# Kernel optimization log

Measured on AMD Instinct MI355X. Metric: run time of the kernel, lower is better.

## Reference

```python
import jax, jax.numpy as jnp
import numpy as np

D_MODEL = 1024
D_K = 64
MAX_LEN = 10000
SCALE = float(np.sqrt(2 * D_K))  # TUPE scale sqrt(2*d_k)


def setup_inputs() -> dict:
    key = jax.random.key(0)
    kq, kk, kv, kpe, kuq, kuk = jax.random.split(key, 6)
    b, s = 4, 2048
    q = jax.random.normal(kq, (b, s, D_MODEL), dtype=jnp.float32)
    k = jax.random.normal(kk, (b, s, D_MODEL), dtype=jnp.float32)
    v = jax.random.normal(kv, (b, s, D_MODEL), dtype=jnp.float32)
    # learned PE, uniform(-0.1, 0.1) as in the source
    pe = jax.random.uniform(kpe, (MAX_LEN, D_MODEL), minval=-0.1, maxval=0.1, dtype=jnp.float32)
    # U_q / U_k: Linear(d_model, d_model, bias=False); store as [in, out] so x @ W matches torch x @ W.T convention after transpose choice
    lim = 1.0 / np.sqrt(D_MODEL)
    Uq = jax.random.uniform(kuq, (D_MODEL, D_MODEL), minval=-lim, maxval=lim, dtype=jnp.float32)
    Uk = jax.random.uniform(kuk, (D_MODEL, D_MODEL), minval=-lim, maxval=lim, dtype=jnp.float32)
    return {"q": q, "k": k, "v": v, "pe": pe, "Uq": Uq, "Uk": Uk}


def reference(q, k, v, pe, Uq, Uk):
    b, len_q, d_model = q.shape
    len_k = k.shape[1]
    # NOTE: source computes scores with FULL q/k (over d_model), not per-head.
    scores = jnp.einsum('bqd,bkd->bqk', q, k)  # [b, lq, lk]
    # TUPE positional attention bias
    q_pe = pe[:len_q] @ Uq  # [lq, d]
    k_pe = pe[:len_k] @ Uk  # [lk, d]
    scores = scores + (q_pe @ k_pe.T)[None, :, :]
    scores = scores / SCALE
    attn = jax.nn.softmax(scores, axis=-1)  # dropout p=0 in eval
    context = jnp.einsum('bqk,bkd->bqd', attn, v)  # [b, lq, d_model]
    # replicate torch transpose(1,2).contiguous().view(b, -1, d_model)
    context = jnp.swapaxes(context, 1, 2).reshape(b, -1, d_model)
    return context, attn
```

## Files before the change

kernel.cpp:

```cpp
#include <hip/hip_runtime.h>
#include <hip/hip_bf16.h>
#include <math.h>

#define BATCH 4
#define SEQ   2048
#define DMODEL 1024

typedef __attribute__((ext_vector_type(8))) short bf16x8;
typedef __attribute__((ext_vector_type(4))) float floatx4;

__device__ __forceinline__ void async_copy16(const void* g, void* lds) {
    __builtin_amdgcn_global_load_lds(
        reinterpret_cast<const unsigned int __attribute__((address_space(1)))*>(
            reinterpret_cast<unsigned long long>(g)),
        reinterpret_cast<unsigned int __attribute__((address_space(3)))*>(
            (unsigned int)reinterpret_cast<unsigned long long>(lds)),
        16, 0, 0);
}

template<bool SPLIT_A, bool HAS_BIAS, bool OUT_TRANS, bool OUT_BF16>
__global__ __launch_bounds__(256, 1)
void mfma_gemm(const __hip_bfloat16* __restrict__ Ah, const __hip_bfloat16* __restrict__ Al,
               const __hip_bfloat16* __restrict__ Bh,
               const float* __restrict__ bias, void* __restrict__ Cvoid,
               int M, int N, int K, float scale,
               long sAb, long sBb, long sCb)
{
    constexpr int NA = SPLIT_A ? 2 : 1;
    __shared__ __align__(16) __hip_bfloat16 sA[NA][128 * 32];
    __shared__ __align__(16) __hip_bfloat16 sB[128 * 32];

    const int bz = blockIdx.z;
    Ah += (long)bz * sAb;
    Bh += (long)bz * sBb;
    if (SPLIT_A) Al += (long)bz * sAb;

    const int row0 = blockIdx.y * 128;
    const int col0 = blockIdx.x * 128;
    const int tid  = threadIdx.x;
    const int wave = tid >> 6;
    const int lane = tid & 63;

    const int srow   = wave * 16 + (lane >> 2);
    const int schunk = (lane & 3) * 8;

    const int wm = (wave >> 1) * 64;
    const int wn = (wave & 1) * 64;
    const int fr = lane & 15;
    const int fk = (lane >> 4) * 8;

    const floatx4 zero = {0.f, 0.f, 0.f, 0.f};
    floatx4 acc[4][4];
    #pragma unroll
    for (int i = 0; i < 4; ++i)
        #pragma unroll
        for (int j = 0; j < 4; ++j) acc[i][j] = zero;

    for (int k0 = 0; k0 < K; k0 += 32) {
        #pragma unroll
        for (int t = 0; t < 2; ++t) {
            const long arow = (long)(row0 + t * 64 + srow);
            const long brow = (long)(col0 + t * 64 + srow);
            const int  soff = (t * 64 + wave * 16) * 32;
            async_copy16(Ah + arow * K + k0 + schunk, &sA[0][soff]);
            async_copy16(Bh + brow * K + k0 + schunk, &sB[soff]);
            if (SPLIT_A)
                async_copy16(Al + arow * K + k0 + schunk, &sA[NA - 1][soff]);
        }
        __syncthreads();

        bf16x8 aH[4], bH[4];
        #pragma unroll
        for (int i = 0; i < 4; ++i) aH[i] = *(const bf16x8*)&sA[0][(wm + i * 16 + fr) * 32 + fk];
        #pragma unroll
        for (int j = 0; j < 4; ++j) bH[j] = *(const bf16x8*)&sB[(wn + j * 16 + fr) * 32 + fk];

        if (SPLIT_A) {
            bf16x8 aL[4];
            #pragma unroll
            for (int i = 0; i < 4; ++i) aL[i] = *(const bf16x8*)&sA[NA - 1][(wm + i * 16 + fr) * 32 + fk];
            #pragma unroll
            for (int i = 0; i < 4; ++i)
                #pragma unroll
                for (int j = 0; j < 4; ++j) {
                    acc[i][j] = __builtin_amdgcn_mfma_f32_16x16x32_bf16(aH[i], bH[j], acc[i][j], 0, 0, 0);
                    acc[i][j] = __builtin_amdgcn_mfma_f32_16x16x32_bf16(aL[i], bH[j], acc[i][j], 0, 0, 0);
                }
        } else {
            #pragma unroll
            for (int i = 0; i < 4; ++i)
                #pragma unroll
                for (int j = 0; j < 4; ++j)
                    acc[i][j] = __builtin_amdgcn_mfma_f32_16x16x32_bf16(aH[i], bH[j], acc[i][j], 0, 0, 0);
        }
        __syncthreads();
    }

    float* Cf = (float*)Cvoid + (long)bz * sCb;
    __hip_bfloat16* Cb = (__hip_bfloat16*)Cvoid + (long)bz * sCb;
    #pragma unroll
    for (int i = 0; i < 4; ++i) {
        #pragma unroll
        for (int r = 0; r < 4; ++r) {
            const int row = row0 + wm + i * 16 + (lane >> 4) * 4 + r;
            #pragma unroll
            for (int j = 0; j < 4; ++j) {
                const int col = col0 + wn + j * 16 + (lane & 15);
                float val = acc[i][j][r];
                if (HAS_BIAS) val += bias[(long)row * N + col];
                val *= scale;
                if (OUT_BF16)       Cb[(long)row * N + col] = __float2bfloat16(val);
                else if (OUT_TRANS) Cf[(long)col * M + row] = val;
                else                Cf[(long)row * N + col] = val;
            }
        }
    }
}

__global__ __launch_bounds__(256)
void convert_bf16_kernel(const float* __restrict__ in, __hip_bfloat16* __restrict__ out, long n)
{
    const long i = ((long)blockIdx.x * 256 + threadIdx.x) * 4;
    if (i >= n) return;
    float va[4];
    *(float4*)va = *(const float4*)(in + i);
    __align__(8) __hip_bfloat16 h[4];
    #pragma unroll
    for (int j = 0; j < 4; ++j) h[j] = __float2bfloat16(va[j]);
    *(uint2*)(out + i) = *(uint2*)h;
}

__global__ __launch_bounds__(256)
void split_convert_kernel(const float* __restrict__ in, __hip_bfloat16* __restrict__ hi,
                          __hip_bfloat16* __restrict__ lo, long n)
{
    const long i = ((long)blockIdx.x * 256 + threadIdx.x) * 4;
    if (i >= n) return;
    float va[4];
    *(float4*)va = *(const float4*)(in + i);
    __align__(8) __hip_bfloat16 h[4], l[4];
    #pragma unroll
    for (int j = 0; j < 4; ++j) {
        h[j] = __float2bfloat16(va[j]);
        l[j] = __float2bfloat16(va[j] - __bfloat162float(h[j]));
    }
    *(uint2*)(hi + i) = *(uint2*)h;
    *(uint2*)(lo + i) = *(uint2*)l;
}

__global__ __launch_bounds__(256)
void transpose_convert_kernel(const float* __restrict__ in, __hip_bfloat16* __restrict__ out,
                              int R, int C, long sIn, long sOut)
{
    in  += (long)blockIdx.z * sIn;
    out += (long)blockIdx.z * sOut;
    __shared__ float t[32][33];
    const int c0 = blockIdx.x * 32, r0 = blockIdx.y * 32;
    for (int i = threadIdx.y; i < 32; i += 8)
        t[i][threadIdx.x] = in[(long)(r0 + i) * C + c0 + threadIdx.x];
    __syncthreads();
    for (int i = threadIdx.y; i < 32; i += 8)
        out[(long)(c0 + i) * R + r0 + threadIdx.x] = __float2bfloat16(t[threadIdx.x][i]);
}

__global__ __launch_bounds__(256)
void softmax_kernel(float* __restrict__ data, __hip_bfloat16* __restrict__ data_bf)
{
    const long row = blockIdx.x;
    float* p = data + row * (long)SEQ;
    __hip_bfloat16* pb = data_bf + row * (long)SEQ;
    const int tid = threadIdx.x;
    const int PER = SEQ / 256;

    float v[PER];
    float m = -1e30f;
    #pragma unroll
    for (int i = 0; i < PER; ++i) {
        v[i] = p[tid + i * 256];
        m = fmaxf(m, v[i]);
    }
    __shared__ float red[256];
    red[tid] = m;
    __syncthreads();
    #pragma unroll
    for (int s = 128; s > 0; s >>= 1) {
        if (tid < s) red[tid] = fmaxf(red[tid], red[tid + s]);
        __syncthreads();
    }
    m = red[0];
    __syncthreads();
    float sum = 0.f;
    #pragma unroll
    for (int i = 0; i < PER; ++i) {
        v[i] = __expf(v[i] - m);
        sum += v[i];
    }
    red[tid] = sum;
    __syncthreads();
    #pragma unroll
    for (int s = 128; s > 0; s >>= 1) {
        if (tid < s) red[tid] += red[tid + s];
        __syncthreads();
    }
    const float inv = 1.0f / red[0];
    #pragma unroll
    for (int i = 0; i < PER; ++i) {
        const float a = v[i] * inv;
        p[tid + i * 256]  = a;
        pb[tid + i * 256] = __float2bfloat16(a);
    }
}

extern "C" void kernel_launch(void* const* d_in, const int* in_sizes, int n_in,
                              void* d_out, int out_size, void* d_ws, size_t ws_size,
                              hipStream_t stream)
{
    const float* q  = (const float*)d_in[0];
    const float* k  = (const float*)d_in[1];
    const float* v  = (const float*)d_in[2];
    const float* pe = (const float*)d_in[3];
    const float* Uq = (const float*)d_in[4];
    const float* Uk = (const float*)d_in[5];

    float* out      = (float*)d_out;
    float* ctx_out  = out;
    float* attn_out = out + (long)BATCH * SEQ * DMODEL;

    const long SD = (long)BATCH * SEQ * DMODEL;
    char* w = (char*)d_ws;
    __hip_bfloat16* q_hi  = (__hip_bfloat16*)w;  w += SD * 2;
    __hip_bfloat16* q_lo  = (__hip_bfloat16*)w;  w += SD * 2;
    __hip_bfloat16* k_bf  = (__hip_bfloat16*)w;  w += SD * 2;
    __hip_bfloat16* pe_bf = (__hip_bfloat16*)w;  w += (long)SEQ * DMODEL * 2;
    __hip_bfloat16* UqT   = (__hip_bfloat16*)w;  w += (long)DMODEL * DMODEL * 2;
    __hip_bfloat16* UkT   = (__hip_bfloat16*)w;  w += (long)DMODEL * DMODEL * 2;
    __hip_bfloat16* qpe_bf= (__hip_bfloat16*)w;  w += (long)SEQ * DMODEL * 2;
    __hip_bfloat16* kpe_bf= (__hip_bfloat16*)w;  w += (long)SEQ * DMODEL * 2;
    float*          biasM = (float*)w;           w += (long)SEQ * SEQ * 4;
    __hip_bfloat16* attn_bf = q_hi;
    __hip_bfloat16* vT      = k_bf;

    const float inv_scale = 1.0f / sqrtf(128.0f);

    convert_bf16_kernel<<<dim3((SEQ * DMODEL) / 4 / 256), 256, 0, stream>>>(pe, pe_bf, (long)SEQ * DMODEL);
    transpose_convert_kernel<<<dim3(DMODEL / 32, DMODEL / 32, 1), dim3(32, 8), 0, stream>>>(
        Uq, UqT, DMODEL, DMODEL, 0, 0);
    transpose_convert_kernel<<<dim3(DMODEL / 32, DMODEL / 32, 1), dim3(32, 8), 0, stream>>>(
        Uk, UkT, DMODEL, DMODEL, 0, 0);
    split_convert_kernel<<<dim3(SD / 4 / 256), 256, 0, stream>>>(q, q_hi, q_lo, SD);
    convert_bf16_kernel<<<dim3(SD / 4 / 256), 256, 0, stream>>>(k, k_bf, SD);

    mfma_gemm<false, false, false, true><<<dim3(DMODEL / 128, SEQ / 128, 2), 256, 0, stream>>>(
        pe_bf, nullptr, UqT, nullptr, qpe_bf, SEQ, DMODEL, DMODEL, 1.0f,
        0, (long)DMODEL * DMODEL, (long)SEQ * DMODEL);

    mfma_gemm<false, false, false, false><<<dim3(SEQ / 128, SEQ / 128, 1), 256, 0, stream>>>(
        qpe_bf, nullptr, kpe_bf, nullptr, biasM, SEQ, SEQ, DMODEL, 1.0f, 0, 0, 0);

    mfma_gemm<true, true, false, false><<<dim3(SEQ / 128, SEQ / 128, BATCH), 256, 0, stream>>>(
        q_hi, q_lo, k_bf, biasM, attn_out, SEQ, SEQ, DMODEL, inv_scale,
        (long)SEQ * DMODEL, (long)SEQ * DMODEL, (long)SEQ * SEQ);

    softmax_kernel<<<dim3(BATCH * SEQ), 256, 0, stream>>>(attn_out, attn_bf);

    transpose_convert_kernel<<<dim3(DMODEL / 32, SEQ / 32, BATCH), dim3(32, 8), 0, stream>>>(
        v, vT, SEQ, DMODEL, (long)SEQ * DMODEL, (long)SEQ * DMODEL);

    mfma_gemm<false, false, true, false><<<dim3(DMODEL / 128, SEQ / 128, BATCH), 256, 0, stream>>>(
        attn_bf, nullptr, vT, nullptr, ctx_out, SEQ, DMODEL, SEQ, 1.0f,
        (long)SEQ * SEQ, (long)SEQ * DMODEL, (long)SEQ * DMODEL);
}
```

Measured before the change: 450.4 us.

## Add 8-wave 256-row tiled GEMM with 4-stage async LDS pipeline for attention GEMMs

Measured after the change: 415.7 us. -7.7%, faster.

```diff
diff --git a/kernel.cpp b/kernel.cpp
--- a/kernel.cpp
+++ b/kernel.cpp
@@ -16,6 +16,160 @@
         reinterpret_cast<unsigned int __attribute__((address_space(3)))*>(
             (unsigned int)reinterpret_cast<unsigned long long>(lds)),
         16, 0, 0);
+}
+
+#define VMCNT(n) asm volatile("s_waitcnt vmcnt(" #n ")" ::: "memory")
+#define SCHED_FENCE() __builtin_amdgcn_sched_barrier(0)
+
+template<bool ASPLIT, int BN, bool HAS_BIAS, bool OUT_TRANS>
+__global__ __launch_bounds__(512, 1)
+void gemm8p(const __hip_bfloat16* __restrict__ A0, const __hip_bfloat16* __restrict__ A1,
+            const __hip_bfloat16* __restrict__ B, const float* __restrict__ bias,
+            float* __restrict__ C, int M, int N, int K, int Kb, float scale,
+            long sAb, long sBb, long sCb)
+{
+    constexpr int BM = 256, BK = 32;
+    constexpr int WN   = BN / 4;
+    constexpr int NF   = WN / 16;
+    constexpr int NPH  = (NF == 4) ? 2 : 1;
+    constexpr int MSUB = 8 / NPH;
+    constexpr int CB   = BN / 128;
+    constexpr int CALLS = 2 + CB;
+
+    __shared__ __align__(16) __hip_bfloat16 sA[4][BM * BK];
+    __shared__ __align__(16) __hip_bfloat16 sB[4][BN * BK];
+
+    const int bz = blockIdx.z;
+    A0 += (long)bz * sAb;
+    if (ASPLIT) A1 += (long)bz * sAb;
+    B += (long)bz * sBb;
+    C += (long)bz * sCb;
+
+    int b = blockIdx.y * gridDim.x + blockIdx.x;
+    const int nwg = gridDim.x * gridDim.y;
+    const int cpx = nwg >> 3;
+    b = (b & 7) * cpx + (b >> 3);
+    const int col0 = (b % gridDim.x) * BN;
+    const int row0 = (b / gridDim.x) * BM;
+
+    const int tid  = threadIdx.x;
+    const int wave = tid >> 6, lane = tid & 63;
+    const int wm = wave >> 2, wn = wave & 3;
+    const int fr = lane & 15, fq = lane >> 4;
+
+    const int NT  = K / BK;
+    const int KA  = ASPLIT ? (K >> 1) : K;
+    const int kbm = Kb - 1;
+
+    const int s_r  = (wave << 4) + (lane >> 2);
+    const int s_c4 = lane & 3;
+
+    auto stageA = [&](int t, int c) {
+        const int lr = (c << 7) + s_r;
+        const int ch = (s_c4 ^ ((lr >> 1) & 3)) << 3;
+        int k0 = t << 5;
+        const __hip_bfloat16* src = A0;
+        if (ASPLIT && k0 >= KA) { src = A1; k0 -= KA; }
+        async_copy16(src + (long)(row0 + lr) * KA + k0 + ch,
+                     &sA[t & 3][((c << 7) + (wave << 4)) * BK]);
+    };
+    auto stageB = [&](int t, int c) {
+        const int lr = (c << 7) + s_r;
+        const int ch = (s_c4 ^ ((lr >> 1) & 3)) << 3;
+        const int k0 = (t << 5) & kbm;
+        async_copy16(B + (long)(col0 + lr) * Kb + k0 + ch,
+                     &sB[t & 3][((c << 7) + (wave << 4)) * BK]);
+    };
+    auto readA = [&](int slot, int i) -> bf16x8 {
+        const int lr = (wm << 7) + (i << 4) + fr;
+        return *(const bf16x8*)&sA[slot][lr * BK + ((fq ^ ((lr >> 1) & 3)) << 3)];
+    };
+    auto readB = [&](int slot, int j) -> bf16x8 {
+        const int lr = wn * WN + (j << 4) + fr;
+        return *(const bf16x8*)&sB[slot][lr * BK + ((fq ^ ((lr >> 1) & 3)) << 3)];
+    };
+
+    floatx4 acc[8][NF];
+    #pragma unroll
+    for (int i = 0; i < 8; ++i)
+        #pragma unroll
+        for (int j = 0; j < NF; ++j) acc[i][j] = (floatx4){0.f, 0.f, 0.f, 0.f};
+
+    #pragma unroll
+    for (int t = 0; t < 3; ++t) {
+        stageA(t, 0); stageA(t, 1);
+        stageB(t, 0); if (CB == 2) stageB(t, 1);
+    }
+    if constexpr (CALLS == 4) { VMCNT(8); } else { VMCNT(6); }
+    __builtin_amdgcn_s_barrier();
+
+    bf16x8 bReg[NF], aReg[MSUB];
+
+    for (int t = 0; t < NT; ++t) {
+        const int slot = t & 3;
+        const bool pf = (t + 3) < NT;
+
+        #pragma unroll
+        for (int j = 0; j < NF; ++j) bReg[j] = readB(slot, j);
+        #pragma unroll
+        for (int i = 0; i < MSUB; ++i) aReg[i] = readA(slot, i);
+        if (pf) {
+            stageA(t + 3, 0); stageA(t + 3, 1);
+            if (NPH == 1) { stageB(t + 3, 0); if (CB == 2) stageB(t + 3, 1); }
+        }
+        SCHED_FENCE();
+        __builtin_amdgcn_s_barrier();
+        __builtin_amdgcn_s_setprio(1);
+        #pragma unroll
+        for (int i = 0; i < MSUB; ++i)
+            #pragma unroll
+            for (int j = 0; j < NF; ++j)
+                acc[i][j] = __builtin_amdgcn_mfma_f32_16x16x32_bf16(aReg[i], bReg[j], acc[i][j], 0, 0, 0);
+        __builtin_amdgcn_s_setprio(0);
+        SCHED_FENCE();
+
+        if constexpr (NPH == 2) {
+            __builtin_amdgcn_s_barrier();
+            #pragma unroll
+            for (int i = 0; i < MSUB; ++i) aReg[i] = readA(slot, MSUB + i);
+            if (pf) { stageB(t + 3, 0); stageB(t + 3, 1); }
+            SCHED_FENCE();
+            __builtin_amdgcn_s_barrier();
+            __builtin_amdgcn_s_setprio(1);
+            #pragma unroll
+            for (int i = 0; i < MSUB; ++i)
+                #pragma unroll
+                for (int j = 0; j < NF; ++j)
+                    acc[MSUB + i][j] = __builtin_amdgcn_mfma_f32_16x16x32_bf16(aReg[i], bReg[j], acc[MSUB + i][j], 0, 0, 0);
+            __builtin_amdgcn_s_setprio(0);
+            SCHED_FENCE();
+        }
+
+        if (t + 1 < NT) {
+            const int ahead = (t + 3 < NT) ? 2 : ((t + 2 < NT) ? 1 : 0);
+            if (ahead == 2)      { if constexpr (CALLS == 4) { VMCNT(8); } else { VMCNT(6); } }
+            else if (ahead == 1) { if constexpr (CALLS == 4) { VMCNT(4); } else { VMCNT(3); } }
+            else                 { VMCNT(0); }
+            __builtin_amdgcn_s_barrier();
+        }
+    }
+
+    #pragma unroll
+    for (int i = 0; i < 8; ++i) {
+        #pragma unroll
+        for (int r = 0; r < 4; ++r) {
+            const int row = row0 + (wm << 7) + (i << 4) + (fq << 2) + r;
+            #pragma unroll
+            for (int j = 0; j < NF; ++j) {
+                const int col = col0 + wn * WN + (j << 4) + fr;
+                float val = acc[i][j][r];
+                if (HAS_BIAS) val += bias[(long)row * N + col];
+                val *= scale;
+                if (OUT_TRANS) C[(long)col * M + row] = val;
+                else           C[(long)row * N + col] = val;
+            }
+        }
+    }
 }
 
 template<bool SPLIT_A, bool HAS_BIAS, bool OUT_TRANS, bool OUT_BF16>
@@ -257,8 +411,8 @@
     mfma_gemm<false, false, false, false><<<dim3(SEQ / 128, SEQ / 128, 1), 256, 0, stream>>>(
         qpe_bf, nullptr, kpe_bf, nullptr, biasM, SEQ, SEQ, DMODEL, 1.0f, 0, 0, 0);
 
-    mfma_gemm<true, true, false, false><<<dim3(SEQ / 128, SEQ / 128, BATCH), 256, 0, stream>>>(
-        q_hi, q_lo, k_bf, biasM, attn_out, SEQ, SEQ, DMODEL, inv_scale,
+    gemm8p<true, 256, true, false><<<dim3(SEQ / 256, SEQ / 256, BATCH), 512, 0, stream>>>(
+        q_hi, q_lo, k_bf, biasM, attn_out, SEQ, SEQ, 2 * DMODEL, DMODEL, inv_scale,
         (long)SEQ * DMODEL, (long)SEQ * DMODEL, (long)SEQ * SEQ);
 
     softmax_kernel<<<dim3(BATCH * SEQ), 256, 0, stream>>>(attn_out, attn_bf);
@@ -266,7 +420,7 @@
     transpose_convert_kernel<<<dim3(DMODEL / 32, SEQ / 32, BATCH), dim3(32, 8), 0, stream>>>(
         v, vT, SEQ, DMODEL, (long)SEQ * DMODEL, (long)SEQ * DMODEL);
 
-    mfma_gemm<false, false, true, false><<<dim3(DMODEL / 128, SEQ / 128, BATCH), 256, 0, stream>>>(
-        attn_bf, nullptr, vT, nullptr, ctx_out, SEQ, DMODEL, SEQ, 1.0f,
+    gemm8p<false, 128, false, true><<<dim3(DMODEL / 128, SEQ / 256, BATCH), 512, 0, stream>>>(
+        attn_bf, nullptr, vT, nullptr, ctx_out, SEQ, DMODEL, SEQ, SEQ, 1.0f,
         (long)SEQ * SEQ, (long)SEQ * DMODEL, (long)SEQ * DMODEL);
 }
```

## Add 8-wave 256-row MFMA GEMM with 4-stage async LDS pipeline for scores and context

Applied to the files above, without the earlier changes.

Result: faster. 406.8 us (-9.7%).

```diff
diff --git a/kernel.cpp b/kernel.cpp
--- a/kernel.cpp
+++ b/kernel.cpp
@@ -16,6 +16,209 @@
         reinterpret_cast<unsigned int __attribute__((address_space(3)))*>(
             (unsigned int)reinterpret_cast<unsigned long long>(lds)),
         16, 0, 0);
+}
+
+#define SCHED_FENCE() __builtin_amdgcn_sched_barrier(0)
+
+
+#define TILE256(T, U) do {                                                      \
+    constexpr int sl  = (U) & 3, sl1 = ((U) + 1) & 3, sl3 = ((U) + 3) & 3;      \
+    constexpr int p = (U) & 1, p1 = ((U) + 1) & 1;                              \
+                               \
+    _Pragma("unroll") for (int i = 0; i < 4; ++i) aH[i] = readA(sl, 4 + i);     \
+    stageA((T) + 3, 0, sl3); stageA((T) + 3, 1, sl3);                           \
+    asm volatile("s_waitcnt vmcnt(6)" ::: "memory");                            \
+    __builtin_amdgcn_s_barrier(); SCHED_FENCE();                                \
+    __builtin_amdgcn_s_setprio(1);                                              \
+    _Pragma("unroll") for (int i = 0; i < 4; ++i)                               \
+      _Pragma("unroll") for (int j = 0; j < 4; ++j)                             \
+        acc[i][j] = __builtin_amdgcn_mfma_f32_16x16x32_bf16(aP[p][i], bP[p][j], acc[i][j], 0, 0, 0); \
+    __builtin_amdgcn_s_setprio(0);                                              \
+                                         \
+    _Pragma("unroll") for (int i = 0; i < 4; ++i) aP[p1][i] = readA(sl1, i);    \
+    _Pragma("unroll") for (int j = 0; j < 4; ++j) bP[p1][j] = readB(sl1, j);    \
+    stageB((T) + 3, 0, sl3); stageB((T) + 3, 1, sl3);                           \
+    asm volatile("s_waitcnt lgkmcnt(8)" ::: "memory");                          \
+    __builtin_amdgcn_s_barrier(); SCHED_FENCE();                                \
+    __builtin_amdgcn_s_setprio(1);                                              \
+    _Pragma("unroll") for (int i = 0; i < 4; ++i)                               \
+      _Pragma("unroll") for (int j = 0; j < 4; ++j)                             \
+        acc[4 + i][j] = __builtin_amdgcn_mfma_f32_16x16x32_bf16(aH[i], bP[p][j], acc[4 + i][j], 0, 0, 0); \
+    __builtin_amdgcn_s_setprio(0);                                              \
+} while (0)
+
+#define DRAIN256(U, LAST) do {                                                  \
+    constexpr int sl = (U) & 3, sl1 = ((U) + 1) & 3;                            \
+    constexpr int p = (U) & 1, p1 = ((U) + 1) & 1;                              \
+    _Pragma("unroll") for (int i = 0; i < 4; ++i) aH[i] = readA(sl, 4 + i);     \
+    _Pragma("unroll") for (int i = 0; i < 4; ++i)                               \
+      _Pragma("unroll") for (int j = 0; j < 4; ++j)                             \
+        acc[i][j] = __builtin_amdgcn_mfma_f32_16x16x32_bf16(aP[p][i], bP[p][j], acc[i][j], 0, 0, 0); \
+    if constexpr (!(LAST)) {                                                    \
+        _Pragma("unroll") for (int i = 0; i < 4; ++i) aP[p1][i] = readA(sl1, i);\
+        _Pragma("unroll") for (int j = 0; j < 4; ++j) bP[p1][j] = readB(sl1, j);\
+    }                                                                           \
+    _Pragma("unroll") for (int i = 0; i < 4; ++i)                               \
+      _Pragma("unroll") for (int j = 0; j < 4; ++j)                             \
+        acc[4 + i][j] = __builtin_amdgcn_mfma_f32_16x16x32_bf16(aH[i], bP[p][j], acc[4 + i][j], 0, 0, 0); \
+} while (0)
+
+#define TILE128(T, U) do {                                                      \
+    constexpr int sl1 = ((U) + 1) & 3, sl3 = ((U) + 3) & 3;                     \
+    constexpr int p = (U) & 1, p1 = ((U) + 1) & 1;                              \
+    asm volatile("s_waitcnt vmcnt(3)" ::: "memory");                            \
+    __builtin_amdgcn_s_barrier(); SCHED_FENCE();                                \
+    _Pragma("unroll") for (int i = 0; i < 8; ++i) aP[p1][i] = readA(sl1, i);    \
+    _Pragma("unroll") for (int j = 0; j < 2; ++j) bP[p1][j] = readB(sl1, j);    \
+    stageA((T) + 3, 0, sl3); stageA((T) + 3, 1, sl3); stageB((T) + 3, 0, sl3);  \
+    asm volatile("s_waitcnt lgkmcnt(10)" ::: "memory");                         \
+    __builtin_amdgcn_s_barrier(); SCHED_FENCE();                                \
+    __builtin_amdgcn_s_setprio(1);                                              \
+    _Pragma("unroll") for (int i = 0; i < 8; ++i)                               \
+      _Pragma("unroll") for (int j = 0; j < 2; ++j)                             \
+        acc[i][j] = __builtin_amdgcn_mfma_f32_16x16x32_bf16(aP[p][i], bP[p][j], acc[i][j], 0, 0, 0); \
+    __builtin_amdgcn_s_setprio(0);                                              \
+} while (0)
+
+#define DRAIN128(U, LAST) do {                                                  \
+    constexpr int sl1 = ((U) + 1) & 3;                                          \
+    constexpr int p = (U) & 1, p1 = ((U) + 1) & 1;                              \
+    if constexpr (!(LAST)) {                                                    \
+        _Pragma("unroll") for (int i = 0; i < 8; ++i) aP[p1][i] = readA(sl1, i);\
+        _Pragma("unroll") for (int j = 0; j < 2; ++j) bP[p1][j] = readB(sl1, j);\
+    }                                                                           \
+    _Pragma("unroll") for (int i = 0; i < 8; ++i)                               \
+      _Pragma("unroll") for (int j = 0; j < 2; ++j)                             \
+        acc[i][j] = __builtin_amdgcn_mfma_f32_16x16x32_bf16(aP[p][i], bP[p][j], acc[i][j], 0, 0, 0); \
+} while (0)
+
+template<bool ASPLIT, int BN, bool HAS_BIAS, int MM, int NN, int KK, int KBB>
+__global__ __launch_bounds__(512, 1)
+void gemm8p(const __hip_bfloat16* __restrict__ A0, const __hip_bfloat16* __restrict__ A1,
+            const __hip_bfloat16* __restrict__ B, const float* __restrict__ bias,
+            float* __restrict__ C, float scale, long sAb, long sBb, long sCb)
+{
+    constexpr int BM = 256, BK = 32;
+    constexpr int NT = KK / BK;
+    constexpr int KA = ASPLIT ? (KK / 2) : KK;
+    constexpr int WN = BN / 4, NF = WN / 16;
+    constexpr int SLOT_A = BM * BK, SLOT_B = BN * BK;
+    constexpr int GX = NN / BN, GY = MM / BM;
+    constexpr int CPX = (GX * GY) / 8;
+    static_assert(NT % 4 == 0 && NT >= 8, "");
+    static_assert((GX * GY) % 8 == 0, "");
+
+    __shared__ __align__(16) __hip_bfloat16 sA[4][SLOT_A];
+    __shared__ __align__(16) __hip_bfloat16 sB[4][SLOT_B];
+
+    const int bz = blockIdx.z;
+    A0 += (long)bz * sAb;
+    if (ASPLIT) A1 += (long)bz * sAb;
+    B += (long)bz * sBb;
+    C += (long)bz * sCb;
+
+    int b = blockIdx.y * GX + blockIdx.x;
+    b = (b & 7) * CPX + (b >> 3);
+    const int col0 = (b % GX) * BN;
+    const int row0 = (b / GX) * BM;
+
+    const int tid  = threadIdx.x;
+    const int wave = tid >> 6, lane = tid & 63;
+    const int wm = wave >> 2, wn = wave & 3;
+    const int fr = lane & 15, fq = lane >> 4;
+    const int swz = (fq ^ ((fr >> 1) & 3)) << 3;
+
+    const int s_r  = (wave << 4) + (lane >> 2);
+    const int s_c4 = lane & 3;
+
+    auto stageA = [&](int t, int c, int sl) {
+        const int lr = (c << 7) + s_r;
+        const int ch = (s_c4 ^ ((lr >> 1) & 3)) << 3;
+        int k0 = t << 5;
+        const __hip_bfloat16* src = A0;
+        if (ASPLIT && k0 >= KA) { src = A1; k0 -= KA; }
+        async_copy16(src + (long)(row0 + lr) * KA + k0 + ch,
+                     &sA[sl][((c << 7) + (wave << 4)) * BK]);
+    };
+    auto stageB = [&](int t, int c, int sl) {
+        const int lr = (c << 7) + s_r;
+        const int ch = (s_c4 ^ ((lr >> 1) & 3)) << 3;
+        const int k0 = (t << 5) & (KBB - 1);
+        async_copy16(B + (long)(col0 + lr) * KBB + k0 + ch,
+                     &sB[sl][((c << 7) + (wave << 4)) * BK]);
+    };
+    auto readA = [&](int sl, int i) -> bf16x8 {
+        return *(const bf16x8*)&sA[sl][((wm << 7) + (i << 4) + fr) * BK + swz];
+    };
+    auto readB = [&](int sl, int j) -> bf16x8 {
+        return *(const bf16x8*)&sB[sl][(wn * WN + (j << 4) + fr) * BK + swz];
+    };
+
+    floatx4 acc[8][NF];
+    #pragma unroll
+    for (int i = 0; i < 8; ++i)
+        #pragma unroll
+        for (int j = 0; j < NF; ++j) acc[i][j] = (floatx4){0.f, 0.f, 0.f, 0.f};
+
+    bf16x8 aP[2][BN == 256 ? 4 : 8];
+    bf16x8 bP[2][NF];
+    bf16x8 aH[BN == 256 ? 4 : 1];
+
+    if constexpr (BN == 256) {
+        stageA(0, 0, 0); stageA(0, 1, 0); stageB(0, 0, 0); stageB(0, 1, 0);
+        stageA(1, 0, 1); stageA(1, 1, 1); stageB(1, 0, 1); stageB(1, 1, 1);
+        stageA(2, 0, 2); stageA(2, 1, 2); stageB(2, 0, 2); stageB(2, 1, 2);
+        asm volatile("s_waitcnt vmcnt(8)" ::: "memory");
+        __builtin_amdgcn_s_barrier(); SCHED_FENCE();
+        #pragma unroll
+        for (int i = 0; i < 4; ++i) aP[0][i] = readA(0, i);
+        #pragma unroll
+        for (int j = 0; j < 4; ++j) bP[0][j] = readB(0, j);
+
+        #pragma unroll 1
+        for (int tt = 0; tt < NT - 4; tt += 4) {
+            TILE256(tt + 0, 0); TILE256(tt + 1, 1); TILE256(tt + 2, 2); TILE256(tt + 3, 3);
+        }
+        TILE256(NT - 4, 0);
+        asm volatile("s_waitcnt vmcnt(0)" ::: "memory");
+        __builtin_amdgcn_s_barrier(); SCHED_FENCE();
+        DRAIN256(1, false); DRAIN256(2, false); DRAIN256(3, true);
+    } else {
+        stageA(0, 0, 0); stageA(0, 1, 0); stageB(0, 0, 0);
+        stageA(1, 0, 1); stageA(1, 1, 1); stageB(1, 0, 1);
+        stageA(2, 0, 2); stageA(2, 1, 2); stageB(2, 0, 2);
+        asm volatile("s_waitcnt vmcnt(6)" ::: "memory");
+        __builtin_amdgcn_s_barrier(); SCHED_FENCE();
+        #pragma unroll
+        for (int i = 0; i < 8; ++i) aP[0][i] = readA(0, i);
+        #pragma unroll
+        for (int j = 0; j < 2; ++j) bP[0][j] = readB(0, j);
+
+        #pragma unroll 1
+        for (int tt = 0; tt < NT - 4; tt += 4) {
+            TILE128(tt + 0, 0); TILE128(tt + 1, 1); TILE128(tt + 2, 2); TILE128(tt + 3, 3);
+        }
+        TILE128(NT - 4, 0);
+        asm volatile("s_waitcnt vmcnt(0)" ::: "memory");
+        __builtin_amdgcn_s_barrier(); SCHED_FENCE();
+        DRAIN128(1, false); DRAIN128(2, false); DRAIN128(3, true);
+    }
+
+    #pragma unroll
+    for (int i = 0; i < 8; ++i) {
+        #pragma unroll
+        for (int r = 0; r < 4; ++r) {
+            const int row = row0 + (wm << 7) + (i << 4) + (fq << 2) + r;
+            #pragma unroll
+            for (int j = 0; j < NF; ++j) {
+                const int col = col0 + wn * WN + (j << 4) + fr;
+                float val = acc[i][j][r];
+                if (HAS_BIAS) val += bias[(long)row * NN + col];
+                val *= scale;
+                C[(long)row * NN + col] = val;
+            }
+        }
+    }
 }
 
 template<bool SPLIT_A, bool HAS_BIAS, bool OUT_TRANS, bool OUT_BF16>
@@ -257,8 +460,9 @@
     mfma_gemm<false, false, false, false><<<dim3(SEQ / 128, SEQ / 128, 1), 256, 0, stream>>>(
         qpe_bf, nullptr, kpe_bf, nullptr, biasM, SEQ, SEQ, DMODEL, 1.0f, 0, 0, 0);
 
-    mfma_gemm<true, true, false, false><<<dim3(SEQ / 128, SEQ / 128, BATCH), 256, 0, stream>>>(
-        q_hi, q_lo, k_bf, biasM, attn_out, SEQ, SEQ, DMODEL, inv_scale,
+    gemm8p<true, 256, true, 2048, 2048, 2048, 1024>
+        <<<dim3(SEQ / 256, SEQ / 256, BATCH), 512, 0, stream>>>(
+        q_hi, q_lo, k_bf, biasM, attn_out, inv_scale,
         (long)SEQ * DMODEL, (long)SEQ * DMODEL, (long)SEQ * SEQ);
 
     softmax_kernel<<<dim3(BATCH * SEQ), 256, 0, stream>>>(attn_out, attn_bf);
@@ -266,7 +470,8 @@
     transpose_convert_kernel<<<dim3(DMODEL / 32, SEQ / 32, BATCH), dim3(32, 8), 0, stream>>>(
         v, vT, SEQ, DMODEL, (long)SEQ * DMODEL, (long)SEQ * DMODEL);
 
-    mfma_gemm<false, false, true, false><<<dim3(DMODEL / 128, SEQ / 128, BATCH), 256, 0, stream>>>(
-        attn_bf, nullptr, vT, nullptr, ctx_out, SEQ, DMODEL, SEQ, 1.0f,
-        (long)SEQ * SEQ, (long)SEQ * DMODEL, (long)SEQ * DMODEL);
-}
+    gemm8p<false, 128, false, 1024, 2048, 2048, 2048>
+        <<<dim3(SEQ / 128, DMODEL / 256, BATCH), 512, 0, stream>>>(
+        vT, nullptr, attn_bf, nullptr, ctx_out, 1.0f,
+        (long)SEQ * DMODEL, (long)SEQ * SEQ, (long)SEQ * DMODEL);
+}
```
